# Kernel tuning notes

Hardware: AMD Instinct MI355X
Metric: run time of the kernel (lower is better)

## Reference

```python
import math
import jax, jax.numpy as jnp
import numpy as np

E = 1024
H = 16
D = E // H  # head_dim = 64
B, T = 4, 2048


def setup_inputs() -> dict:
    key = jax.random.key(0)
    ks = jax.random.split(key, 9)
    s = 1.0 / math.sqrt(E)
    inp = {
        "x": jax.random.normal(ks[0], (B, T, E), dtype=jnp.float32),
        "Wq": jax.random.uniform(ks[1], (E, E), jnp.float32, -s, s),
        "bq": jax.random.uniform(ks[2], (E,), jnp.float32, -s, s),
        "Wk": jax.random.uniform(ks[3], (E, E), jnp.float32, -s, s),
        "bk": jax.random.uniform(ks[4], (E,), jnp.float32, -s, s),
        "Wv": jax.random.uniform(ks[5], (E, E), jnp.float32, -s, s),
        "bv": jax.random.uniform(ks[6], (E,), jnp.float32, -s, s),
        "Wo": jax.random.uniform(ks[7], (E, E), jnp.float32, -s, s),
        "bo": jax.random.uniform(ks[8], (E,), jnp.float32, -s, s),
    }
    return inp


def reference(x, Wq, bq, Wk, bk, Wv, bv, Wo, bo):
    # Linear projections (torch Linear: y = x @ W.T + b)
    q = x @ Wq.T + bq
    k = x @ Wk.T + bk
    v = x @ Wv.T + bv
    # [B, T, E] -> [B, H, T, D]
    def split_heads(t):
        return t.reshape(B, T, H, D).transpose(0, 2, 1, 3)
    q, k, v = split_heads(q), split_heads(k), split_heads(v)
    # scaled dot-product attention; note scale uses head_dim (attention(self.head_dim))
    scores = jnp.einsum("bhqd,bhkd->bhqk", q, k) / math.sqrt(D)
    attn = jax.nn.softmax(scores, axis=-1)
    out = jnp.einsum("bhqk,bhkd->bhqd", attn, v)
    out = out.transpose(0, 2, 1, 3).reshape(B, T, E)
    return out @ Wo.T + bo
```

## Files before the change

### kernel.cpp

```cpp
#include <hip/hip_runtime.h>

typedef short bh8 __attribute__((ext_vector_type(8)));
typedef short bh4 __attribute__((ext_vector_type(4)));
typedef float f4 __attribute__((ext_vector_type(4)));
typedef unsigned int u32;
typedef u32 u32x2 __attribute__((ext_vector_type(2)));

#if __has_builtin(__builtin_amdgcn_exp2f)
#define EXP2(x) __builtin_amdgcn_exp2f(x)
#else
#define EXP2(x) exp2f(x)
#endif

__device__ __forceinline__ short f2bf(float f) {
  unsigned u = __float_as_uint(f);
  u += 0x7FFFu + ((u >> 16) & 1u);
  return (short)(u >> 16);
}

__device__ __forceinline__ void async16(const void* g, void* l) {
  __builtin_amdgcn_global_load_lds((const __attribute__((address_space(1))) void*)g,
                                   (__attribute__((address_space(3))) void*)l, 16, 0, 0);
}

__global__ void cvt_kernel(const float* __restrict__ in, short* __restrict__ out, int n4) {
  int i = blockIdx.x * blockDim.x + threadIdx.x;
  if (i < n4) {
    f4 v = *(const f4*)(in + (size_t)i * 4);
    bh4 o;
    o[0] = f2bf(v[0]); o[1] = f2bf(v[1]); o[2] = f2bf(v[2]); o[3] = f2bf(v[3]);
    *(bh4*)(out + (size_t)i * 4) = o;
  }
}

__global__ void cvt_w4(const float* __restrict__ w0, const float* __restrict__ w1,
                       const float* __restrict__ w2, const float* __restrict__ w3,
                       short* __restrict__ out, int n4_per) {
  const float* in = blockIdx.y == 0 ? w0 : blockIdx.y == 1 ? w1 : blockIdx.y == 2 ? w2 : w3;
  short* o = out + (size_t)blockIdx.y * (size_t)n4_per * 4;
  int i = blockIdx.x * blockDim.x + threadIdx.x;
  if (i < n4_per) {
    f4 v = *(const f4*)(in + (size_t)i * 4);
    bh4 q;
    q[0] = f2bf(v[0]); q[1] = f2bf(v[1]); q[2] = f2bf(v[2]); q[3] = f2bf(v[3]);
    *(bh4*)(o + (size_t)i * 4) = q;
  }
}

template <typename OutT, bool BROW>
__device__ __forceinline__ void gemm_body(const short* __restrict__ A, const short* __restrict__ Bw,
                                          const float* __restrict__ bias, OutT* __restrict__ C,
                                          int m0, int n0, int N, int K, float scale,
                                          short* a_lds, short* b_lds) {
  const int t = threadIdx.x;
  const int lane = t & 63, wave = t >> 6, quad = lane >> 4, l15 = lane & 15;
  const int mw = (wave >> 1) * 64, nw = (wave & 1) * 64;

  f4 acc[4][4];
#pragma unroll
  for (int i = 0; i < 4; ++i)
#pragma unroll
    for (int j = 0; j < 4; ++j) acc[i][j] = (f4){0.f, 0.f, 0.f, 0.f};

  for (int k0 = 0; k0 < K; k0 += 32) {
#pragma unroll
    for (int i = 0; i < 2; ++i) {
      int c = i * 256 + t;
      int m = c >> 2;
      int kq = (c & 3) ^ ((m >> 1) & 3);
      const short* ga = A + (size_t)(m0 + m) * K + k0 + kq * 8;
      const short* gb = Bw + (size_t)(n0 + m) * K + k0 + kq * 8;
      async16(ga, (char*)a_lds + (i * 256 + wave * 64) * 16);
      async16(gb, (char*)b_lds + (i * 256 + wave * 64) * 16);
    }
    __syncthreads();
    bh8 af[4], bfr[4];
#pragma unroll
    for (int ms = 0; ms < 4; ++ms) {
      int m = mw + ms * 16 + l15;
      int pos = m * 4 + (quad ^ ((m >> 1) & 3));
      af[ms] = *(const bh8*)(a_lds + pos * 8);
    }
#pragma unroll
    for (int ns = 0; ns < 4; ++ns) {
      int n = nw + ns * 16 + l15;
      int pos = n * 4 + (quad ^ ((n >> 1) & 3));
      bfr[ns] = *(const bh8*)(b_lds + pos * 8);
    }
#pragma unroll
    for (int ms = 0; ms < 4; ++ms)
#pragma unroll
      for (int ns = 0; ns < 4; ++ns)
        acc[ms][ns] = __builtin_amdgcn_mfma_f32_16x16x32_bf16(af[ms], bfr[ns], acc[ms][ns], 0, 0, 0);
    __syncthreads();
  }
#pragma unroll
  for (int ns = 0; ns < 4; ++ns) {
    int col = n0 + nw + ns * 16 + l15;
    float bcol = BROW ? 0.f : bias[col & 1023];
#pragma unroll
    for (int ms = 0; ms < 4; ++ms) {
      int row = m0 + mw + ms * 16 + quad * 4;
      float brow = BROW ? bias[row & 1023] : 0.f;
#pragma unroll
      for (int r = 0; r < 4; ++r) {
        float bv = BROW ? bias[(row + r) & 1023] : bcol;
        float v = (acc[ms][ns][r] + bv) * scale;
        if (sizeof(OutT) == 2)
          ((short*)C)[(size_t)(row + r) * N + col] = f2bf(v);
        else
          ((float*)C)[(size_t)(row + r) * N + col] = v;
      }
      (void)brow;
    }
  }
}

__global__ void gemm_qkv(const short* __restrict__ xb, const short* __restrict__ W3,
                         const float* __restrict__ bq, const float* __restrict__ bk,
                         const float* __restrict__ bv,
                         short* __restrict__ Qo, short* __restrict__ Ko, short* __restrict__ VTo,
                         float qscale) {
  __shared__ __align__(16) short a_lds[128 * 32];
  __shared__ __align__(16) short b_lds[128 * 32];
  const int which = blockIdx.x >> 3;
  if (which == 2) {
    const short* Wv = W3 + (size_t)2 * 1024 * 1024;
    gemm_body<short, true>(Wv, xb, bv, VTo, (blockIdx.x & 7) * 128, blockIdx.y * 128,
                           8192, 1024, 1.0f, a_lds, b_lds);
  } else {
    const short* Bw = W3 + (size_t)which * 1024 * 1024;
    const float* bias = which == 0 ? bq : bk;
    short* C = which == 0 ? Qo : Ko;
    float scale = which == 0 ? qscale : 1.0f;
    gemm_body<short, false>(xb, Bw, bias, C, blockIdx.y * 128, (blockIdx.x & 7) * 128,
                            1024, 1024, scale, a_lds, b_lds);
  }
}

__global__ void gemm_bt_f32(const short* __restrict__ A, const short* __restrict__ Bw,
                            const float* __restrict__ bias, float* __restrict__ C) {
  __shared__ __align__(16) short a_lds[128 * 32];
  __shared__ __align__(16) short b_lds[128 * 32];
  gemm_body<float, false>(A, Bw, bias, C, blockIdx.y * 128, blockIdx.x * 128, 1024, 1024, 1.0f,
                          a_lds, b_lds);
}

__global__ void attn_kernel(const short* __restrict__ Qb, const short* __restrict__ Kb,
                            const short* __restrict__ VTb, short* __restrict__ AO) {
  __shared__ __align__(16) short k_lds[64 * 64];
  __shared__ __align__(16) short vt_lds[64 * 64];
  __shared__ __align__(16) short p_lds[4][32 * 72];
  const int t = threadIdx.x, lane = t & 63, wave = t >> 6, quad = lane >> 4, l15 = lane & 15;
  const int bh = blockIdx.y, b = bh >> 4, h = bh & 15;
  const int q0 = blockIdx.x * 128;
  const size_t baseq = ((size_t)b * 2048) * 1024 + (size_t)h * 64;
  const size_t basev = ((size_t)h * 64) * 8192 + (size_t)b * 2048;

  bh8 qf[2][2];
#pragma unroll
  for (int mi = 0; mi < 2; ++mi)
#pragma unroll
    for (int ks = 0; ks < 2; ++ks)
      qf[mi][ks] = *(const bh8*)(Qb + baseq + (size_t)(q0 + wave * 32 + mi * 16 + l15) * 1024 + ks * 32 + quad * 8);

  f4 O[2][4];
  float l_part[2] = {0.f, 0.f};
#pragma unroll
  for (int mi = 0; mi < 2; ++mi)
#pragma unroll
    for (int di = 0; di < 4; ++di) O[mi][di] = (f4){0.f, 0.f, 0.f, 0.f};

  for (int kt = 0; kt < 2048; kt += 64) {
    __syncthreads();
#pragma unroll
    for (int i = 0; i < 2; ++i) {
      int c = i * 256 + t;
      int kk = c >> 3;
      int dq = (c & 7) ^ (kk & 7);
      async16(Kb + baseq + (size_t)(kt + kk) * 1024 + dq * 8,
              (char*)k_lds + (i * 256 + wave * 64) * 16);
    }
#pragma unroll
    for (int i = 0; i < 2; ++i) {
      int c = i * 256 + t;
      int d = c >> 3;
      int kc = (c & 7) ^ (d & 7);
      async16(VTb + basev + (size_t)d * 8192 + kt + kc * 8,
              (char*)vt_lds + (i * 256 + wave * 64) * 16);
    }
    __syncthreads();

    f4 ST[4][2];
#pragma unroll
    for (int mK = 0; mK < 4; ++mK) {
      int key = mK * 16 + l15;
      bh8 ka0 = *(const bh8*)(k_lds + (key * 8 + (quad ^ (key & 7))) * 8);
      bh8 ka1 = *(const bh8*)(k_lds + (key * 8 + ((quad + 4) ^ (key & 7))) * 8);
#pragma unroll
      for (int mi = 0; mi < 2; ++mi) {
        f4 s = (f4){-16.f, -16.f, -16.f, -16.f};
        s = __builtin_amdgcn_mfma_f32_16x16x32_bf16(ka0, qf[mi][0], s, 0, 0, 0);
        s = __builtin_amdgcn_mfma_f32_16x16x32_bf16(ka1, qf[mi][1], s, 0, 0, 0);
        ST[mK][mi] = s;
      }
    }

#pragma unroll
    for (int mi = 0; mi < 2; ++mi) {
      float lp = 0.f;
#pragma unroll
      for (int mK = 0; mK < 4; ++mK) {
        float p0 = EXP2(ST[mK][mi][0]);
        float p1 = EXP2(ST[mK][mi][1]);
        float p2 = EXP2(ST[mK][mi][2]);
        float p3 = EXP2(ST[mK][mi][3]);
        lp += (p0 + p1) + (p2 + p3);
        u32 d0 = __builtin_amdgcn_perm(__float_as_uint(p1), __float_as_uint(p0), 0x07060302u);
        u32 d1 = __builtin_amdgcn_perm(__float_as_uint(p3), __float_as_uint(p2), 0x07060302u);
        u32x2 dd = {d0, d1};
        *(u32x2*)(&p_lds[wave][(mi * 16 + l15) * 72 + mK * 16 + quad * 4]) = dd;
      }
      l_part[mi] += lp;
    }

    bh8 pa[2][2];
#pragma unroll
    for (int mi = 0; mi < 2; ++mi)
#pragma unroll
      for (int ks = 0; ks < 2; ++ks)
        pa[mi][ks] = *(const bh8*)(&p_lds[wave][(mi * 16 + l15) * 72 + ks * 32 + quad * 8]);
#pragma unroll
    for (int di = 0; di < 4; ++di) {
      int d = di * 16 + l15;
      bh8 vb0 = *(const bh8*)(vt_lds + (d * 8 + (quad ^ (d & 7))) * 8);
      bh8 vb1 = *(const bh8*)(vt_lds + (d * 8 + ((quad + 4) ^ (d & 7))) * 8);
#pragma unroll
      for (int mi = 0; mi < 2; ++mi) {
        f4 o = O[mi][di];
        o = __builtin_amdgcn_mfma_f32_16x16x32_bf16(pa[mi][0], vb0, o, 0, 0, 0);
        o = __builtin_amdgcn_mfma_f32_16x16x32_bf16(pa[mi][1], vb1, o, 0, 0, 0);
        O[mi][di] = o;
      }
    }
  }

#pragma unroll
  for (int mi = 0; mi < 2; ++mi) {
    float l0 = l_part[mi];
    l0 += __shfl_xor(l0, 16);
    l0 += __shfl_xor(l0, 32);
    float rl[4];
#pragma unroll
    for (int r = 0; r < 4; ++r) {
      float lb = __shfl(l0, quad * 4 + r);
      rl[r] = __builtin_amdgcn_rcpf(lb);
    }
#pragma unroll
    for (int di = 0; di < 4; ++di)
#pragma unroll
      for (int r = 0; r < 4; ++r) {
        int row = q0 + wave * 32 + mi * 16 + quad * 4 + r;
        AO[baseq + (size_t)row * 1024 + di * 16 + l15] = f2bf(O[mi][di][r] * rl[r]);
      }
  }
}

extern "C" void kernel_launch(void* const* d_in, const int* in_sizes, int n_in,
                              void* d_out, int out_size, void* d_ws, size_t ws_size,
                              hipStream_t stream) {
  const float* x  = (const float*)d_in[0];
  const float* Wq = (const float*)d_in[1];
  const float* bq = (const float*)d_in[2];
  const float* Wk = (const float*)d_in[3];
  const float* bk = (const float*)d_in[4];
  const float* Wv = (const float*)d_in[5];
  const float* bv = (const float*)d_in[6];
  const float* Wo = (const float*)d_in[7];
  const float* bo = (const float*)d_in[8];
  float* out = (float*)d_out;

  const int M = 8192, E = 1024;
  const size_t NX = (size_t)M * E;
  const size_t NW = (size_t)E * E;

  short* ws  = (short*)d_ws;
  short* xb  = ws;
  short* wqb = xb + NX;
  short* wob = wqb + 3 * NW;
  short* qb  = wob + NW;
  short* kb  = qb + NX;
  short* vt  = kb + NX;
  short* aob = xb;

  cvt_kernel<<<dim3((unsigned)(NX / 1024)), 256, 0, stream>>>(x, xb, (int)(NX / 4));
  cvt_w4<<<dim3((unsigned)(NW / 1024), 4), 256, 0, stream>>>(Wq, Wk, Wv, Wo, wqb, (int)(NW / 4));

  const float qscale = 0.18033688011112042f;
  gemm_qkv<<<dim3(24, 64), 256, 0, stream>>>(xb, wqb, bq, bk, bv, qb, kb, vt, qscale);

  attn_kernel<<<dim3(16, 64), 256, 0, stream>>>(qb, kb, vt, aob);

  gemm_bt_f32<<<dim3(8, 64), 256, 0, stream>>>(aob, wob, bo, out);
}
```

Measured before the change: 280.7 us.

## Double-buffer K/V tiles in attention and raise priority around MFMA blocks

```diff
diff --git a/kernel.cpp b/kernel.cpp
--- a/kernel.cpp
+++ b/kernel.cpp
@@ -148,8 +148,8 @@
 
 __global__ void attn_kernel(const short* __restrict__ Qb, const short* __restrict__ Kb,
                             const short* __restrict__ VTb, short* __restrict__ AO) {
-  __shared__ __align__(16) short k_lds[64 * 64];
-  __shared__ __align__(16) short vt_lds[64 * 64];
+  __shared__ __align__(16) short k_lds[2][64 * 64];
+  __shared__ __align__(16) short vt_lds[2][64 * 64];
   __shared__ __align__(16) short p_lds[4][32 * 72];
   const int t = threadIdx.x, lane = t & 63, wave = t >> 6, quad = lane >> 4, l15 = lane & 15;
   const int bh = blockIdx.y, b = bh >> 4, h = bh & 15;
@@ -171,15 +171,14 @@
 #pragma unroll
     for (int di = 0; di < 4; ++di) O[mi][di] = (f4){0.f, 0.f, 0.f, 0.f};
 
-  for (int kt = 0; kt < 2048; kt += 64) {
-    __syncthreads();
+  auto stage = [&](int buf, int kt) {
 #pragma unroll
     for (int i = 0; i < 2; ++i) {
       int c = i * 256 + t;
       int kk = c >> 3;
       int dq = (c & 7) ^ (kk & 7);
       async16(Kb + baseq + (size_t)(kt + kk) * 1024 + dq * 8,
-              (char*)k_lds + (i * 256 + wave * 64) * 16);
+              (char*)(k_lds[buf]) + (i * 256 + wave * 64) * 16);
     }
 #pragma unroll
     for (int i = 0; i < 2; ++i) {
@@ -187,16 +186,29 @@
       int d = c >> 3;
       int kc = (c & 7) ^ (d & 7);
       async16(VTb + basev + (size_t)d * 8192 + kt + kc * 8,
-              (char*)vt_lds + (i * 256 + wave * 64) * 16);
-    }
-    __syncthreads();
+              (char*)(vt_lds[buf]) + (i * 256 + wave * 64) * 16);
+    }
+  };
+
+  stage(0, 0);
+  asm volatile("s_waitcnt vmcnt(0)" ::: "memory");
+  __builtin_amdgcn_s_barrier();
+  asm volatile("" ::: "memory");
+
+  int cur = 0;
+  for (int kt = 0; kt < 2048; kt += 64) {
+    if (kt + 64 < 2048) stage(cur ^ 1, kt + 64);
+
+    const short* kl = k_lds[cur];
+    const short* vl = vt_lds[cur];
 
     f4 ST[4][2];
+    __builtin_amdgcn_s_setprio(1);
 #pragma unroll
     for (int mK = 0; mK < 4; ++mK) {
       int key = mK * 16 + l15;
-      bh8 ka0 = *(const bh8*)(k_lds + (key * 8 + (quad ^ (key & 7))) * 8);
-      bh8 ka1 = *(const bh8*)(k_lds + (key * 8 + ((quad + 4) ^ (key & 7))) * 8);
+      bh8 ka0 = *(const bh8*)(kl + (key * 8 + (quad ^ (key & 7))) * 8);
+      bh8 ka1 = *(const bh8*)(kl + (key * 8 + ((quad + 4) ^ (key & 7))) * 8);
 #pragma unroll
       for (int mi = 0; mi < 2; ++mi) {
         f4 s = (f4){-16.f, -16.f, -16.f, -16.f};
@@ -205,6 +217,7 @@
         ST[mK][mi] = s;
       }
     }
+    __builtin_amdgcn_s_setprio(0);
 
 #pragma unroll
     for (int mi = 0; mi < 2; ++mi) {
@@ -230,11 +243,12 @@
 #pragma unroll
       for (int ks = 0; ks < 2; ++ks)
         pa[mi][ks] = *(const bh8*)(&p_lds[wave][(mi * 16 + l15) * 72 + ks * 32 + quad * 8]);
+    __builtin_amdgcn_s_setprio(1);
 #pragma unroll
     for (int di = 0; di < 4; ++di) {
       int d = di * 16 + l15;
-      bh8 vb0 = *(const bh8*)(vt_lds + (d * 8 + (quad ^ (d & 7))) * 8);
-      bh8 vb1 = *(const bh8*)(vt_lds + (d * 8 + ((quad + 4) ^ (d & 7))) * 8);
+      bh8 vb0 = *(const bh8*)(vl + (d * 8 + (quad ^ (d & 7))) * 8);
+      bh8 vb1 = *(const bh8*)(vl + (d * 8 + ((quad + 4) ^ (d & 7))) * 8);
 #pragma unroll
       for (int mi = 0; mi < 2; ++mi) {
         f4 o = O[mi][di];
@@ -243,6 +257,12 @@
         O[mi][di] = o;
       }
     }
+    __builtin_amdgcn_s_setprio(0);
+
+    asm volatile("s_waitcnt vmcnt(0)" ::: "memory");
+    __builtin_amdgcn_s_barrier();
+    asm volatile("" ::: "memory");
+    cur ^= 1;
   }
 
 #pragma unroll
```

New measurement: 288.5 us. +2.8%, slower.
